# Kernel optimization log

Hardware: AMD Instinct MI355X
Metric: run time of the kernel (lower is better)

Reference implementation:

```python
import jax, jax.numpy as jnp
import numpy as np

B, C, N, K, OUT = 4, 128, 8192, 20, 128


def setup_inputs() -> dict:
    key = jax.random.key(0)
    k1, k2, k3 = jax.random.split(key, 3)
    x = jax.random.normal(k1, (B, C, N), dtype=jnp.float32)
    W = jax.random.normal(k2, (OUT, 2 * C), dtype=jnp.float32) * 0.02  # 1x1 conv weight over 2C edge channels
    b = jnp.zeros((OUT,), dtype=jnp.float32)
    return {"x": x, "W": W, "b": b}


def _knn_idx(x, k):
    # x: [B, C, N]; pairwise_distance = -||xi - xj||^2 (larger = closer)
    inner = -2.0 * jnp.einsum('bcn,bcm->bnm', x, x)          # [B,N,N]
    xx = jnp.sum(x * x, axis=1)                               # [B,N]
    pd = -xx[:, :, None] - inner - xx[:, None, :]             # [B,N,N]
    return jax.lax.top_k(pd, k)[1]                            # [B,N,k] int32


def reference(x, W, b):
    k = K
    idx = _knn_idx(x, k)                                      # [B,N,k]
    xt = jnp.transpose(x, (0, 2, 1))                          # [B,N,C]
    nbr = jax.vmap(lambda xb, ib: xb[ib])(xt, idx)            # [B,N,k,C] gather
    center = jnp.broadcast_to(xt[:, :, None, :], nbr.shape)   # [B,N,k,C]
    # torch: cat((x, x - feature), dim=3)
    edge = jnp.concatenate([center, center - nbr], axis=-1)   # [B,N,k,2C]
    # 1x1 Conv2d over channel dim + ReLU
    h = jnp.einsum('bnkc,oc->bonk', edge, W) + b[None, :, None, None]
    h = jax.nn.relu(h)
    # aggregate over neighbors (EdgeConv max pooling)
    return jnp.max(h, axis=-1)                                # [B,OUT,N]
```

## Files before the change

kernel.cpp:

```cpp
#include <hip/hip_runtime.h>
#include <float.h>

#define Bz   4
#define Cz   128
#define Nz   8192
#define Kz   20
#define OUTz 128

__global__ __launch_bounds__(256) void xx_kernel(const float* __restrict__ x,
                                                 float* __restrict__ xx) {
    int t = blockIdx.x * 256 + threadIdx.x;
    int b = t >> 13;
    int n = t & (Nz - 1);
    const float* xp = x + (size_t)b * Cz * Nz + n;
    float s = 0.f;
#pragma unroll 8
    for (int c = 0; c < Cz; ++c) {
        float v = xp[(size_t)c * Nz];
        s = fmaf(v, v, s);
    }
    xx[t] = s;
}

__global__ __launch_bounds__(256, 3) void knn_kernel(const float* __restrict__ x,
                                                     const float* __restrict__ xxg,
                                                     int* __restrict__ idxout) {
    const int b   = blockIdx.y;
    const int qi0 = blockIdx.x * 64;

    __shared__ __align__(16) float xq[128 * 64];
    __shared__ __align__(16) float xs[32 * 128];

    const int tid  = threadIdx.x;
    const int tx   = tid & 15;
    const int ty   = tid >> 4;
    const int lane = tid & 63;
    const int wave = tid >> 6;

    const float* xb = x + (size_t)b * Cz * Nz;

    {
        int li = tid & 63;
        int c0 = tid >> 6;
#pragma unroll
        for (int rep = 0; rep < 32; ++rep) {
            int c = c0 + rep * 4;
            xq[c * 64 + li] = xb[(size_t)c * Nz + qi0 + li];
        }
    }

    float tv[Kz];
    int   ti[Kz];
#pragma unroll
    for (int s = 0; s < Kz; ++s) { tv[s] = -FLT_MAX; ti[s] = 0; }
    float wv = -FLT_MAX;
    int wslot = 0;
    const int myrow = wave * 16 + lane;

    const int aoff  = ty * 4;
    const int b0off = tx * 4;
    const int b1off = 64 + tx * 4;

    for (int kt = 0; kt < Nz / 128; ++kt) {
        const int kj0 = kt * 128;
        float acc[4][8];
#pragma unroll
        for (int di = 0; di < 4; ++di)
#pragma unroll
            for (int dj = 0; dj < 8; ++dj) acc[di][dj] = 0.f;

#pragma unroll
        for (int cc = 0; cc < 4; ++cc) {
            __syncthreads();
#pragma unroll
            for (int r = 0; r < 4; ++r) {
                int f4 = tid + 256 * r;
                int c  = f4 >> 5;
                int k4 = (f4 & 31) * 4;
                *(float4*)&xs[c * 128 + k4] =
                    *(const float4*)&xb[(size_t)(cc * 32 + c) * Nz + kj0 + k4];
            }
            __syncthreads();
#pragma unroll 8
            for (int c = 0; c < 32; ++c) {
                float4 a = *(const float4*)&xq[(cc * 32 + c) * 64 + aoff];
                float4 p = *(const float4*)&xs[c * 128 + b0off];
                float4 q = *(const float4*)&xs[c * 128 + b1off];
                float av[4] = {a.x, a.y, a.z, a.w};
                float pv[4] = {p.x, p.y, p.z, p.w};
                float qv[4] = {q.x, q.y, q.z, q.w};
#pragma unroll
                for (int di = 0; di < 4; ++di) {
#pragma unroll
                    for (int dj = 0; dj < 4; ++dj) {
                        acc[di][dj]     = fmaf(av[di], pv[dj], acc[di][dj]);
                        acc[di][4 + dj] = fmaf(av[di], qv[dj], acc[di][4 + dj]);
                    }
                }
            }
        }
        __syncthreads();

#pragma unroll
        for (int h = 0; h < 2; ++h) {
            {
                float4 xxv = *(const float4*)&xxg[b * Nz + kj0 + h * 64 + tx * 4];
                float xxa[4] = {xxv.x, xxv.y, xxv.z, xxv.w};
#pragma unroll
                for (int di = 0; di < 4; ++di) {
                    int r = ty * 4 + di;
                    float4 w;
                    w.x = 2.f * acc[di][h * 4 + 0] - xxa[0];
                    w.y = 2.f * acc[di][h * 4 + 1] - xxa[1];
                    w.z = 2.f * acc[di][h * 4 + 2] - xxa[2];
                    w.w = 2.f * acc[di][h * 4 + 3] - xxa[3];
                    *(float4*)&xs[r * 64 + ((tx * 4 + 4 * r) & 63)] = w;
                }
            }
            __syncthreads();

            if (lane < 16) {
                unsigned long long pm = 0ull;
#pragma unroll
                for (int g = 0; g < 16; ++g) {
                    float4 v = *(const float4*)&xs[myrow * 64 + ((g * 4 + 4 * myrow) & 63)];
                    if (v.x > wv) pm |= 1ull << (4 * g + 0);
                    if (v.y > wv) pm |= 1ull << (4 * g + 1);
                    if (v.z > wv) pm |= 1ull << (4 * g + 2);
                    if (v.w > wv) pm |= 1ull << (4 * g + 3);
                }
                while (pm) {
                    int j = __ffsll(pm) - 1;
                    pm &= pm - 1;
                    float s = xs[myrow * 64 + ((j + 4 * myrow) & 63)];
                    if (s > wv) {
                        int gj = kj0 + h * 64 + j;
#pragma unroll
                        for (int s2 = 0; s2 < Kz; ++s2) {
                            bool hit = (s2 == wslot);
                            tv[s2] = hit ? s : tv[s2];
                            ti[s2] = hit ? gj : ti[s2];
                        }
                        wv = tv[0]; wslot = 0;
#pragma unroll
                        for (int s2 = 1; s2 < Kz; ++s2) {
                            if (tv[s2] < wv) { wv = tv[s2]; wslot = s2; }
                        }
                    }
                }
            }
            __syncthreads();
        }
    }

    if (lane < 16) {
        size_t base = ((size_t)b * Nz + qi0 + myrow) * Kz;
#pragma unroll
        for (int s = 0; s < Kz; ++s) idxout[base + s] = ti[s];
    }
}

__global__ __launch_bounds__(256) void feat_kernel(const float* __restrict__ x,
                                                   const float* __restrict__ W,
                                                   const float* __restrict__ bias,
                                                   float* __restrict__ Y) {
    const int gp0 = blockIdx.x * 64;
    const int b   = gp0 >> 13;
    const int n0  = gp0 & (Nz - 1);
    const int o0  = blockIdx.y * 64;

    __shared__ __align__(16) float xt[128 * 64];
    __shared__ __align__(16) float wt[128 * 64];

    const int tid = threadIdx.x;
    const int tx  = tid & 15;
    const int ty  = tid >> 4;

    {
        int li = tid & 63;
        int c0 = tid >> 6;
        const float* xbp = x + (size_t)b * Cz * Nz + n0;
#pragma unroll
        for (int rep = 0; rep < 32; ++rep) {
            int c = c0 + rep * 4;
            xt[c * 64 + li] = xbp[(size_t)c * Nz + li];
        }
    }
    {
        int lo = tid & 63;
        int c0 = tid >> 6;
        int oo = o0 + lo;
#pragma unroll
        for (int rep = 0; rep < 32; ++rep) {
            int c = c0 + rep * 4;
            float w;
            if (oo < 128) w = W[oo * 256 + c] + W[oo * 256 + 128 + c];
            else          w = W[(oo - 128) * 256 + 128 + c];
            wt[c * 64 + lo] = w;
        }
    }
    __syncthreads();

    float acc[4][4];
#pragma unroll
    for (int di = 0; di < 4; ++di)
#pragma unroll
        for (int dj = 0; dj < 4; ++dj) acc[di][dj] = 0.f;

    const int aoff = ty * 4;
    const int boff = tx * 4;
#pragma unroll 8
    for (int c = 0; c < 128; ++c) {
        float4 a  = *(const float4*)&xt[c * 64 + aoff];
        float4 ww = *(const float4*)&wt[c * 64 + boff];
        float av[4] = {a.x, a.y, a.z, a.w};
        float wvv[4] = {ww.x, ww.y, ww.z, ww.w};
#pragma unroll
        for (int di = 0; di < 4; ++di)
#pragma unroll
            for (int dj = 0; dj < 4; ++dj)
                acc[di][dj] = fmaf(av[di], wvv[dj], acc[di][dj]);
    }

    float4 bv = make_float4(0.f, 0.f, 0.f, 0.f);
    if (o0 < 128) bv = *(const float4*)&bias[o0 + tx * 4];
#pragma unroll
    for (int di = 0; di < 4; ++di) {
        float4 r;
        r.x = acc[di][0] + bv.x;
        r.y = acc[di][1] + bv.y;
        r.z = acc[di][2] + bv.z;
        r.w = acc[di][3] + bv.w;
        *(float4*)&Y[(size_t)(gp0 + ty * 4 + di) * 256 + o0 + tx * 4] = r;
    }
}

__global__ __launch_bounds__(256) void gather_kernel(const int* __restrict__ idxg,
                                                     const float* __restrict__ Y,
                                                     float* __restrict__ out) {
    const int gp0 = blockIdx.x * 64;
    const int b   = gp0 >> 13;
    const int n0  = gp0 & (Nz - 1);

    __shared__ int lidx[64 * 21];
    const int tid = threadIdx.x;
    for (int t = tid; t < 64 * Kz; t += 256) {
        int p = t / Kz, j = t - p * Kz;
        lidx[p * 21 + j] = idxg[(size_t)(gp0 + p) * Kz + j];
    }
    __syncthreads();

    const int p  = tid & 63;
    const int o0 = (tid >> 6) * 32;

    float mn[32];
#pragma unroll
    for (int q = 0; q < 32; ++q) mn[q] = FLT_MAX;

    for (int j = 0; j < Kz; ++j) {
        int m = lidx[p * 21 + j];
        const float4* vr =
            (const float4*)(Y + (size_t)(b * Nz + m) * 256 + 128 + o0);
#pragma unroll
        for (int q = 0; q < 8; ++q) {
            float4 v4 = vr[q];
            mn[4 * q + 0] = fminf(mn[4 * q + 0], v4.x);
            mn[4 * q + 1] = fminf(mn[4 * q + 1], v4.y);
            mn[4 * q + 2] = fminf(mn[4 * q + 2], v4.z);
            mn[4 * q + 3] = fminf(mn[4 * q + 3], v4.w);
        }
    }

    const float4* ur = (const float4*)(Y + (size_t)(gp0 + p) * 256 + o0);
#pragma unroll
    for (int q = 0; q < 8; ++q) {
        float4 u4 = ur[q];
        float r0 = fmaxf(u4.x - mn[4 * q + 0], 0.f);
        float r1 = fmaxf(u4.y - mn[4 * q + 1], 0.f);
        float r2 = fmaxf(u4.z - mn[4 * q + 2], 0.f);
        float r3 = fmaxf(u4.w - mn[4 * q + 3], 0.f);
        size_t ob = ((size_t)b * OUTz + o0 + 4 * q) * Nz + n0 + p;
        out[ob + 0 * Nz] = r0;
        out[ob + 1 * Nz] = r1;
        out[ob + 2 * Nz] = r2;
        out[ob + 3 * Nz] = r3;
    }
}

extern "C" void kernel_launch(void* const* d_in, const int* in_sizes, int n_in,
                              void* d_out, int out_size, void* d_ws, size_t ws_size,
                              hipStream_t stream) {
    const float* x    = (const float*)d_in[0];
    const float* W    = (const float*)d_in[1];
    const float* bias = (const float*)d_in[2];
    float* out = (float*)d_out;

    char* ws = (char*)d_ws;
    float* xx  = (float*)ws;
    int*   idx = (int*)(ws + (1 << 17));
    float* Y   = (float*)(ws + (4 << 20));

    xx_kernel<<<dim3(Bz * Nz / 256), dim3(256), 0, stream>>>(x, xx);

    knn_kernel<<<dim3(Nz / 64, Bz), dim3(256), 0, stream>>>(x, xx, idx);

    feat_kernel<<<dim3(Bz * Nz / 64, 4), dim3(256), 0, stream>>>(x, W, bias, Y);

    gather_kernel<<<dim3(Bz * Nz / 64), dim3(256), 0, stream>>>(idx, Y, out);
}
```

Baseline: 1.346 ms.

## Double-buffer KNN tile loads via registers and parallelize candidate mask scan across wave

The KNN kernel now prefetches the next 32-channel chunk of the key tile into registers while computing on the current one, alternating between two shared buffers so only one barrier is needed per chunk. The two 64-column halves of the distance tile are written at once into the two buffers, which removes a barrier round. The threshold comparison that builds the candidate bitmask is spread across all 64 lanes and merged with shuffles, instead of running on only 16 lanes. In exchange the kernel uses more shared memory and registers, and launch bounds drop from 3 to 2 blocks per CU, which lowers occupancy.

```diff
diff --git a/kernel.cpp b/kernel.cpp
--- a/kernel.cpp
+++ b/kernel.cpp
@@ -22,14 +22,15 @@
     xx[t] = s;
 }
 
-__global__ __launch_bounds__(256, 3) void knn_kernel(const float* __restrict__ x,
+__global__ __launch_bounds__(256, 2) void knn_kernel(const float* __restrict__ x,
                                                      const float* __restrict__ xxg,
                                                      int* __restrict__ idxout) {
     const int b   = blockIdx.y;
     const int qi0 = blockIdx.x * 64;
 
     __shared__ __align__(16) float xq[128 * 64];
-    __shared__ __align__(16) float xs[32 * 128];
+    __shared__ __align__(16) float bufA[32 * 128];
+    __shared__ __align__(16) float bufB[32 * 128];
 
     const int tid  = threadIdx.x;
     const int tx   = tid & 15;
@@ -56,13 +57,42 @@
     float wv = -FLT_MAX;
     int wslot = 0;
     const int myrow = wave * 16 + lane;
+    const int srow  = wave * 16 + (lane & 15);
+    const int spart = lane >> 4;
 
     const int aoff  = ty * 4;
     const int b0off = tx * 4;
     const int b1off = 64 + tx * 4;
 
+    float4 st0[4], st1[4];
+
+#define LOADCHUNK(dst, kj0, cc)                                               \
+    {                                                                         \
+        _Pragma("unroll")                                                     \
+        for (int r = 0; r < 4; ++r) {                                         \
+            int f4 = tid + 256 * r;                                           \
+            int c  = f4 >> 5;                                                 \
+            int k4 = (f4 & 31) * 4;                                           \
+            dst[r] = *(const float4*)&xb[(size_t)((cc) * 32 + c) * Nz + (kj0) + k4]; \
+        }                                                                     \
+    }
+
+#define WRITECHUNK(src, buf)                                                  \
+    {                                                                         \
+        _Pragma("unroll")                                                     \
+        for (int r = 0; r < 4; ++r) {                                         \
+            int f4 = tid + 256 * r;                                           \
+            int c  = f4 >> 5;                                                 \
+            int k4 = (f4 & 31) * 4;                                           \
+            *(float4*)&buf[c * 128 + k4] = src[r];                            \
+        }                                                                     \
+    }
+
+    LOADCHUNK(st0, 0, 0);
+
     for (int kt = 0; kt < Nz / 128; ++kt) {
-        const int kj0 = kt * 128;
+        const int kj0  = kt * 128;
+        const int kj0n = ((kt + 1) & (Nz / 128 - 1)) * 128;
         float acc[4][8];
 #pragma unroll
         for (int di = 0; di < 4; ++di)
@@ -71,21 +101,20 @@
 
 #pragma unroll
         for (int cc = 0; cc < 4; ++cc) {
+            float* buf = (cc & 1) ? bufB : bufA;
+            if (cc & 1) { WRITECHUNK(st1, buf); } else { WRITECHUNK(st0, buf); }
             __syncthreads();
-#pragma unroll
-            for (int r = 0; r < 4; ++r) {
-                int f4 = tid + 256 * r;
-                int c  = f4 >> 5;
-                int k4 = (f4 & 31) * 4;
-                *(float4*)&xs[c * 128 + k4] =
-                    *(const float4*)&xb[(size_t)(cc * 32 + c) * Nz + kj0 + k4];
-            }
-            __syncthreads();
+            if (cc < 3) {
+                if (cc & 1) { LOADCHUNK(st0, kj0, cc + 1); }
+                else        { LOADCHUNK(st1, kj0, cc + 1); }
+            } else {
+                LOADCHUNK(st0, kj0n, 0);
+            }
 #pragma unroll 8
             for (int c = 0; c < 32; ++c) {
                 float4 a = *(const float4*)&xq[(cc * 32 + c) * 64 + aoff];
-                float4 p = *(const float4*)&xs[c * 128 + b0off];
-                float4 q = *(const float4*)&xs[c * 128 + b1off];
+                float4 p = *(const float4*)&buf[c * 128 + b0off];
+                float4 q = *(const float4*)&buf[c * 128 + b1off];
                 float av[4] = {a.x, a.y, a.z, a.w};
                 float pv[4] = {p.x, p.y, p.z, p.w};
                 float qv[4] = {q.x, q.y, q.z, q.w};
@@ -101,56 +130,81 @@
         }
         __syncthreads();
 
-#pragma unroll
-        for (int h = 0; h < 2; ++h) {
-            {
-                float4 xxv = *(const float4*)&xxg[b * Nz + kj0 + h * 64 + tx * 4];
-                float xxa[4] = {xxv.x, xxv.y, xxv.z, xxv.w};
-#pragma unroll
-                for (int di = 0; di < 4; ++di) {
-                    int r = ty * 4 + di;
-                    float4 w;
-                    w.x = 2.f * acc[di][h * 4 + 0] - xxa[0];
-                    w.y = 2.f * acc[di][h * 4 + 1] - xxa[1];
-                    w.z = 2.f * acc[di][h * 4 + 2] - xxa[2];
-                    w.w = 2.f * acc[di][h * 4 + 3] - xxa[3];
-                    *(float4*)&xs[r * 64 + ((tx * 4 + 4 * r) & 63)] = w;
-                }
-            }
-            __syncthreads();
+        {
+            float4 xx0 = *(const float4*)&xxg[b * Nz + kj0 + tx * 4];
+            float4 xx1 = *(const float4*)&xxg[b * Nz + kj0 + 64 + tx * 4];
+            float xxa0[4] = {xx0.x, xx0.y, xx0.z, xx0.w};
+            float xxa1[4] = {xx1.x, xx1.y, xx1.z, xx1.w};
+#pragma unroll
+            for (int di = 0; di < 4; ++di) {
+                int r = ty * 4 + di;
+                int ro = (4 * tx + 4 * r) & 63;
+                float4 w0, w1;
+                w0.x = 2.f * acc[di][0] - xxa0[0];
+                w0.y = 2.f * acc[di][1] - xxa0[1];
+                w0.z = 2.f * acc[di][2] - xxa0[2];
+                w0.w = 2.f * acc[di][3] - xxa0[3];
+                w1.x = 2.f * acc[di][4] - xxa1[0];
+                w1.y = 2.f * acc[di][5] - xxa1[1];
+                w1.z = 2.f * acc[di][6] - xxa1[2];
+                w1.w = 2.f * acc[di][7] - xxa1[3];
+                *(float4*)&bufA[r * 64 + ro] = w0;
+                *(float4*)&bufB[r * 64 + ro] = w1;
+            }
+        }
+        __syncthreads();
+
+        {
+            float wvb = __shfl(wv, lane & 15);
+            unsigned m0 = 0, m1 = 0;
+#pragma unroll
+            for (int g = 0; g < 4; ++g) {
+                int col = 16 * spart + 4 * g;
+                int ad  = srow * 64 + ((col + 4 * srow) & 63);
+                float4 v0 = *(const float4*)&bufA[ad];
+                float4 v1 = *(const float4*)&bufB[ad];
+                m0 |= (unsigned)(v0.x > wvb) << (4 * g + 0);
+                m0 |= (unsigned)(v0.y > wvb) << (4 * g + 1);
+                m0 |= (unsigned)(v0.z > wvb) << (4 * g + 2);
+                m0 |= (unsigned)(v0.w > wvb) << (4 * g + 3);
+                m1 |= (unsigned)(v1.x > wvb) << (4 * g + 0);
+                m1 |= (unsigned)(v1.y > wvb) << (4 * g + 1);
+                m1 |= (unsigned)(v1.z > wvb) << (4 * g + 2);
+                m1 |= (unsigned)(v1.w > wvb) << (4 * g + 3);
+            }
+            unsigned long long f0 = (unsigned long long)m0 << (16 * spart);
+            unsigned long long f1 = (unsigned long long)m1 << (16 * spart);
+            f0 |= __shfl_xor(f0, 16); f0 |= __shfl_xor(f0, 32);
+            f1 |= __shfl_xor(f1, 16); f1 |= __shfl_xor(f1, 32);
 
             if (lane < 16) {
-                unsigned long long pm = 0ull;
-#pragma unroll
-                for (int g = 0; g < 16; ++g) {
-                    float4 v = *(const float4*)&xs[myrow * 64 + ((g * 4 + 4 * myrow) & 63)];
-                    if (v.x > wv) pm |= 1ull << (4 * g + 0);
-                    if (v.y > wv) pm |= 1ull << (4 * g + 1);
-                    if (v.z > wv) pm |= 1ull << (4 * g + 2);
-                    if (v.w > wv) pm |= 1ull << (4 * g + 3);
-                }
-                while (pm) {
-                    int j = __ffsll(pm) - 1;
-                    pm &= pm - 1;
-                    float s = xs[myrow * 64 + ((j + 4 * myrow) & 63)];
-                    if (s > wv) {
-                        int gj = kj0 + h * 64 + j;
-#pragma unroll
-                        for (int s2 = 0; s2 < Kz; ++s2) {
-                            bool hit = (s2 == wslot);
-                            tv[s2] = hit ? s : tv[s2];
-                            ti[s2] = hit ? gj : ti[s2];
-                        }
-                        wv = tv[0]; wslot = 0;
-#pragma unroll
-                        for (int s2 = 1; s2 < Kz; ++s2) {
-                            if (tv[s2] < wv) { wv = tv[s2]; wslot = s2; }
+#pragma unroll
+                for (int h = 0; h < 2; ++h) {
+                    unsigned long long pm = h ? f1 : f0;
+                    const float* sb = h ? bufB : bufA;
+                    while (pm) {
+                        int j = __ffsll(pm) - 1;
+                        pm &= pm - 1;
+                        float s = sb[myrow * 64 + ((j + 4 * myrow) & 63)];
+                        if (s > wv) {
+                            int gj = kj0 + h * 64 + j;
+#pragma unroll
+                            for (int s2 = 0; s2 < Kz; ++s2) {
+                                bool hit = (s2 == wslot);
+                                tv[s2] = hit ? s : tv[s2];
+                                ti[s2] = hit ? gj : ti[s2];
+                            }
+                            wv = tv[0]; wslot = 0;
+#pragma unroll
+                            for (int s2 = 1; s2 < Kz; ++s2) {
+                                if (tv[s2] < wv) { wv = tv[s2]; wslot = s2; }
+                            }
                         }
                     }
                 }
             }
-            __syncthreads();
-        }
+        }
+        __syncthreads();
     }
 
     if (lane < 16) {
@@ -158,6 +212,8 @@
 #pragma unroll
         for (int s = 0; s < Kz; ++s) idxout[base + s] = ti[s];
     }
+#undef LOADCHUNK
+#undef WRITECHUNK
 }
 
 __global__ __launch_bounds__(256) void feat_kernel(const float* __restrict__ x,
```

Measured after the change: 1.329 ms. Within noise of the previous version (-1.3%).
